# Optimization experiments

Measured on AMD Instinct MI355X. Metric: run time of the kernel, lower is better.

## Reference

```python
import jax, jax.numpy as jnp
import numpy as np

N_NODE = 100_000
N_EDGE = 1_000_000
N_QUERY = 256
N_REL = 200  # embedding table has 2*N_REL+1 = 401 rows
IN_DIM = 64
OUT_DIM = 64
ATTN_DIM = 64


def setup_inputs() -> dict:
    key = jax.random.key(0)
    ks = jax.random.split(key, 12)
    r_idx = jax.random.randint(ks[0], (N_EDGE,), 0, N_QUERY)
    rel = jax.random.randint(ks[1], (N_EDGE,), 0, 2 * N_REL + 1)
    sub = jax.random.randint(ks[2], (N_EDGE,), 0, N_NODE)
    obj = jax.random.randint(ks[3], (N_EDGE,), 0, N_NODE)
    zeros = jnp.zeros((N_EDGE,), dtype=jnp.int32)
    # columns: [r_idx, _, rel, _, sub, obj] matching edges[:,0],[:,2],[:,4],[:,5]
    edges = jnp.stack([r_idx, zeros, rel, zeros, sub, obj], axis=1)
    return {
        "q_sub": jax.random.randint(ks[4], (N_QUERY,), 0, N_NODE),
        "q_rel": jax.random.randint(ks[5], (N_QUERY,), 0, 2 * N_REL + 1),
        "hidden": jax.random.normal(ks[6], (N_NODE, IN_DIM), dtype=jnp.float32),
        "edges": edges,
        "n_node": N_NODE,
        "rela_embed": jax.random.normal(ks[7], (2 * N_REL + 1, IN_DIM), dtype=jnp.float32) * 0.1,
        "Ws": jax.random.normal(ks[8], (IN_DIM, ATTN_DIM), dtype=jnp.float32) * (IN_DIM ** -0.5),
        "Wr": jax.random.normal(ks[9], (IN_DIM, ATTN_DIM), dtype=jnp.float32) * (IN_DIM ** -0.5),
        "Wqr": jax.random.normal(ks[10], (IN_DIM, ATTN_DIM), dtype=jnp.float32) * (IN_DIM ** -0.5),
        "Wqr_b": jnp.zeros((ATTN_DIM,), dtype=jnp.float32),
        "w_alpha_w": jax.random.normal(ks[11], (ATTN_DIM, 1), dtype=jnp.float32) * (ATTN_DIM ** -0.5),
        "w_alpha_b": jnp.zeros((1,), dtype=jnp.float32),
        "W_h": jax.random.normal(jax.random.fold_in(key, 99), (IN_DIM, OUT_DIM), dtype=jnp.float32) * (IN_DIM ** -0.5),
    }


def reference(q_sub, q_rel, hidden, edges, n_node, rela_embed, Ws, Wr, Wqr,
              Wqr_b, w_alpha_w, w_alpha_b, W_h):
    sub = edges[:, 4]
    rel = edges[:, 2]
    obj = edges[:, 5]
    r_idx = edges[:, 0]

    hs = hidden[sub]                    # [E, in_dim] gather
    hr = rela_embed[rel]                # [E, in_dim]
    h_qr = rela_embed[q_rel][r_idx]     # [E, in_dim]

    message = hs + hr                   # [E, in_dim]

    attn = jax.nn.relu(hs @ Ws + hr @ Wr + (h_qr @ Wqr + Wqr_b))  # [E, attn_dim]
    alpha_temp = attn @ w_alpha_w + w_alpha_b                      # [E, 1]
    alpha = jax.nn.sigmoid(alpha_temp)                             # [E, 1]

    message = alpha * message
    message_agg = jax.ops.segment_sum(message, obj, num_segments=n_node)  # [n_node, in_dim]
    hidden_new = message_agg @ W_h      # act is identity (default)
    return hidden_new, alpha, message, obj, alpha_temp
```

## Files before the change

kernel.cpp:

```cpp
#include <hip/hip_runtime.h>
#include <hip/hip_bf16.h>
#include <hip/hip_fp16.h>
#include <cstddef>


typedef float    f32x4 __attribute__((ext_vector_type(4)));
typedef _Float16 f16x8 __attribute__((ext_vector_type(8)));

#define NT_STORE(p, v) __builtin_nontemporal_store((v), (p))

__global__ void fused_pre_kernel(const float* __restrict__ hidden,
                                 const float* __restrict__ Ws,
                                 _Float16* __restrict__ packed, int nnode,
                                 const float* __restrict__ rela,
                                 const float* __restrict__ Wr,
                                 const float* __restrict__ Wqr,
                                 const float* __restrict__ Wqr_b,
                                 const int* __restrict__ q_rel,
                                 _Float16* __restrict__ Br16,
                                 _Float16* __restrict__ Cq16,
                                 _Float16* __restrict__ rela16,
                                 int nrel, int nq,
                                 _Float16* __restrict__ agg,
                                 int mmB, int relB, int zB) {
    __shared__ float W1[64][64];
    __shared__ float W2[64][64];
    int bid = blockIdx.x;
    int tid = threadIdx.x;

    if (bid < mmB) {
        for (int i = tid; i < 4096; i += 256) W1[i >> 6][i & 63] = Ws[i];
        __syncthreads();
        int col = tid & 63, r4 = tid >> 6;
        for (long row = (long)bid * 4 + r4; row < nnode; row += (long)mmB * 4) {
            float xv  = hidden[row * 64 + col];
            float acc = 0.0f;
#pragma unroll
            for (int k = 0; k < 64; ++k)
                acc = fmaf(__shfl(xv, k, 64), W1[k][col], acc);
            packed[row * 128 + col]      = (_Float16)xv;
            packed[row * 128 + 64 + col] = (_Float16)acc;
        }
    } else if (bid < mmB + relB) {
        for (int i = tid; i < 4096; i += 256) {
            W1[i >> 6][i & 63] = Wr[i];
            W2[i >> 6][i & 63] = Wqr[i];
        }
        __syncthreads();
        int col = tid & 63, r4 = tid >> 6;
        int row = (bid - mmB) * 4 + r4;
        int total = nrel + nq;
        if (row < total) {
            if (row < nrel) {
                float xv  = rela[(size_t)row * 64 + col];
                float acc = 0.0f;
#pragma unroll
                for (int k = 0; k < 64; ++k)
                    acc = fmaf(__shfl(xv, k, 64), W1[k][col], acc);
                Br16[(size_t)row * 64 + col]   = (_Float16)acc;
                rela16[(size_t)row * 64 + col] = (_Float16)xv;
            } else {
                int q  = row - nrel;
                int rr = q_rel[q];
                float xv  = rela[(size_t)rr * 64 + col];
                float acc = Wqr_b[col];
#pragma unroll
                for (int k = 0; k < 64; ++k)
                    acc = fmaf(__shfl(xv, k, 64), W2[k][col], acc);
                Cq16[(size_t)q * 64 + col] = (_Float16)acc;
            }
        }
    } else {
        size_t n16 = (size_t)nnode * 8;
        size_t i = (size_t)(bid - mmB - relB) * 256 + tid;
        size_t stride = (size_t)zB * 256;
        f32x4 z = {0.f, 0.f, 0.f, 0.f};
        for (; i < n16; i += stride)
            __builtin_nontemporal_store(z, (f32x4*)agg + i);
    }
}

__global__ void edge_kernel(const int* __restrict__ edges,
                            const _Float16* __restrict__ packed,
                            const _Float16* __restrict__ rela16,
                            const _Float16* __restrict__ Br16,
                            const _Float16* __restrict__ Cq16,
                            const float* __restrict__ w_alpha_w,
                            const float* __restrict__ w_alpha_b,
                            _Float16* __restrict__ agg,
                            float* __restrict__ out_alpha,
                            float* __restrict__ out_message,
                            float* __restrict__ out_obj,
                            float* __restrict__ out_alpha_temp,
                            int nedge) {
    __shared__ __align__(16) _Float16 sm[4][8][64];
    int tid  = threadIdx.x;
    int wv   = tid >> 6;
    int lane = tid & 63;
    int g    = lane >> 3;
    int s    = lane & 7;
    long e0  = ((long)blockIdx.x * 4 + wv) * 8;
    if ((long)blockIdx.x * 32 >= nedge) return;
    long e   = e0 + g;
    bool valid = (e < nedge);

    int md = 0;
    long mbase = e0 * 6;
    if (lane < 48 && (mbase + lane) < (long)nedge * 6) md = edges[mbase + lane];
    int r_idx = __shfl(md, g * 6 + 0, 64);
    int rel   = __shfl(md, g * 6 + 2, 64);
    int sub   = __shfl(md, g * 6 + 4, 64);
    int obj   = __shfl(md, g * 6 + 5, 64);
    if (!valid) { r_idx = 0; rel = 0; sub = 0; obj = 0; }

    const f16x8 hh = *(const f16x8*)(packed + (size_t)sub * 128 + s * 8);
    const f16x8 hw = *(const f16x8*)(packed + (size_t)sub * 128 + 64 + s * 8);
    const f16x8 br = *(const f16x8*)(Br16   + (size_t)rel   * 64 + s * 8);
    const f16x8 cq = *(const f16x8*)(Cq16   + (size_t)r_idx * 64 + s * 8);
    const f16x8 rv = *(const f16x8*)(rela16 + (size_t)rel   * 64 + s * 8);
    const f32x4 wa0 = *(const f32x4*)(w_alpha_w + s * 8);
    const f32x4 wa1 = *(const f32x4*)(w_alpha_w + s * 8 + 4);

    float dot = 0.0f;
#pragma unroll
    for (int j = 0; j < 8; ++j) {
        float a  = fmaxf((float)hw[j] + (float)br[j] + (float)cq[j], 0.0f);
        float wj = (j < 4) ? wa0[j] : wa1[j - 4];
        dot = fmaf(a, wj, dot);
    }
    dot += __shfl_xor(dot, 1, 64);
    dot += __shfl_xor(dot, 2, 64);
    dot += __shfl_xor(dot, 4, 64);

    float at    = dot + w_alpha_b[0];
    float alpha = 1.0f / (1.0f + __expf(-at));

    float m[8];
#pragma unroll
    for (int j = 0; j < 8; ++j)
        m[j] = alpha * ((float)hh[j] + (float)rv[j]);

    if (valid) {
        f32x4 m0 = {m[0], m[1], m[2], m[3]};
        f32x4 m1 = {m[4], m[5], m[6], m[7]};
        __builtin_nontemporal_store(m0, (f32x4*)(out_message + e * 64 + s * 8));
        __builtin_nontemporal_store(m1, (f32x4*)(out_message + e * 64 + s * 8 + 4));
        if (s == 0) {
            NT_STORE(&out_alpha[e], alpha);
            NT_STORE(&out_obj[e], (float)obj);
            NT_STORE(&out_alpha_temp[e], at);
        }
    }

    f16x8 mh;
#pragma unroll
    for (int j = 0; j < 8; ++j) mh[j] = (_Float16)m[j];
    *(f16x8*)&sm[wv][g][s * 8] = mh;
    __syncthreads();
#pragma unroll
    for (int i = 0; i < 4; ++i) {
        int k = 2 * i + (lane >> 5);
        int h = lane & 31;
        if (e0 + k < nedge) {
            __half2 v = *(__half2*)&sm[wv][k][h * 2];
            int ok = __shfl(obj, k * 8, 64);
            unsafeAtomicAdd((__half2*)(agg + (size_t)ok * 64) + h, v);
        }
    }
}

__global__ void matmul64_f16_kernel(const _Float16* __restrict__ X,
                                    const float* __restrict__ W,
                                    float* __restrict__ Y, int nrows) {
    __shared__ float Wl[64][64];
    int tid = threadIdx.x;
    for (int i = tid; i < 4096; i += 256) Wl[i >> 6][i & 63] = W[i];
    __syncthreads();
    int col = tid & 63;
    int r4  = tid >> 6;
    for (long row = (long)blockIdx.x * 4 + r4; row < nrows;
         row += (long)gridDim.x * 4) {
        float xv  = (float)X[row * 64 + col];
        float acc = 0.0f;
#pragma unroll
        for (int k = 0; k < 64; ++k)
            acc = fmaf(__shfl(xv, k, 64), Wl[k][col], acc);
        NT_STORE(&Y[row * 64 + col], acc);
    }
}

extern "C" void kernel_launch(void* const* d_in, const int* in_sizes, int n_in,
                              void* d_out, int out_size, void* d_ws, size_t ws_size,
                              hipStream_t stream) {
    const int*   q_rel     = (const int*)d_in[1];
    const float* hidden    = (const float*)d_in[2];
    const int*   edges     = (const int*)d_in[3];
    const float* rela      = (const float*)d_in[5];
    const float* Ws        = (const float*)d_in[6];
    const float* Wr        = (const float*)d_in[7];
    const float* Wqr       = (const float*)d_in[8];
    const float* Wqr_b     = (const float*)d_in[9];
    const float* w_alpha_w = (const float*)d_in[10];
    const float* w_alpha_b = (const float*)d_in[11];
    const float* W_h       = (const float*)d_in[12];

    const int n_node = in_sizes[2] / 64;
    const int n_edge = in_sizes[3] / 6;
    const int n_rel  = in_sizes[5] / 64;
    const int n_q    = in_sizes[1];

    float* out            = (float*)d_out;
    float* out_hidden_new = out;
    float* out_alpha      = out + (size_t)n_node * 64;
    float* out_message    = out_alpha + n_edge;
    float* out_obj        = out_message + (size_t)n_edge * 64;
    float* out_alpha_temp = out_obj + n_edge;

    _Float16* packed = (_Float16*)d_ws;
    _Float16* agg    = packed + (size_t)n_node * 128;
    _Float16* Br16   = agg + (size_t)n_node * 64;
    _Float16* Cq16   = Br16 + (size_t)n_rel * 64;
    _Float16* rela16 = Cq16 + (size_t)n_q * 64;

    const int mmB  = 2048;
    const int relB = (n_rel + n_q + 3) / 4;
    const int zB   = 512;
    fused_pre_kernel<<<mmB + relB + zB, 256, 0, stream>>>(
        hidden, Ws, packed, n_node,
        rela, Wr, Wqr, Wqr_b, q_rel, Br16, Cq16, rela16, n_rel, n_q,
        agg, mmB, relB, zB);

    {
        int grid = (n_edge + 31) / 32;
        edge_kernel<<<grid, 256, 0, stream>>>(edges, packed, rela16, Br16, Cq16,
                                              w_alpha_w, w_alpha_b, agg,
                                              out_alpha, out_message, out_obj,
                                              out_alpha_temp, n_edge);
    }

    matmul64_f16_kernel<<<2048, 256, 0, stream>>>(agg, W_h, out_hidden_new,
                                                  n_node);
}
```

Measured before the change: 266.8 us.

## Drop edge-kernel block barrier, split rel/query precompute, add dual accumulators

Removes the __syncthreads between the per-wave LDS staging write and the atomic scatter reads in the edge kernel. This relies on each wave only reading its own sm[wv] slice. The Wr and Wqr projections now run in separate block ranges, so each block stages a single 64x64 weight tile and the second shared array is gone. All three 64-wide matvec loops use two independent accumulators for extra ILP. The number of projection blocks for hidden@Ws doubles. Skipping the barrier is correct only if same-wave LDS write-to-read ordering holds, which the code does not enforce explicitly.

```diff
diff --git a/kernel.cpp b/kernel.cpp
--- a/kernel.cpp
+++ b/kernel.cpp
@@ -22,9 +22,8 @@
                                  _Float16* __restrict__ rela16,
                                  int nrel, int nq,
                                  _Float16* __restrict__ agg,
-                                 int mmB, int relB, int zB) {
+                                 int mmB, int brB, int cqB, int zB) {
     __shared__ float W1[64][64];
-    __shared__ float W2[64][64];
     int bid = blockIdx.x;
     int tid = threadIdx.x;
 
@@ -34,45 +33,50 @@
         int col = tid & 63, r4 = tid >> 6;
         for (long row = (long)bid * 4 + r4; row < nnode; row += (long)mmB * 4) {
             float xv  = hidden[row * 64 + col];
-            float acc = 0.0f;
-#pragma unroll
-            for (int k = 0; k < 64; ++k)
-                acc = fmaf(__shfl(xv, k, 64), W1[k][col], acc);
+            float a0 = 0.0f, a1 = 0.0f;
+#pragma unroll
+            for (int k = 0; k < 64; k += 2) {
+                a0 = fmaf(__shfl(xv, k, 64),     W1[k][col],     a0);
+                a1 = fmaf(__shfl(xv, k + 1, 64), W1[k + 1][col], a1);
+            }
             packed[row * 128 + col]      = (_Float16)xv;
-            packed[row * 128 + 64 + col] = (_Float16)acc;
-        }
-    } else if (bid < mmB + relB) {
-        for (int i = tid; i < 4096; i += 256) {
-            W1[i >> 6][i & 63] = Wr[i];
-            W2[i >> 6][i & 63] = Wqr[i];
-        }
+            packed[row * 128 + 64 + col] = (_Float16)(a0 + a1);
+        }
+    } else if (bid < mmB + brB) {
+        for (int i = tid; i < 4096; i += 256) W1[i >> 6][i & 63] = Wr[i];
         __syncthreads();
         int col = tid & 63, r4 = tid >> 6;
         int row = (bid - mmB) * 4 + r4;
-        int total = nrel + nq;
-        if (row < total) {
-            if (row < nrel) {
-                float xv  = rela[(size_t)row * 64 + col];
-                float acc = 0.0f;
-#pragma unroll
-                for (int k = 0; k < 64; ++k)
-                    acc = fmaf(__shfl(xv, k, 64), W1[k][col], acc);
-                Br16[(size_t)row * 64 + col]   = (_Float16)acc;
-                rela16[(size_t)row * 64 + col] = (_Float16)xv;
-            } else {
-                int q  = row - nrel;
-                int rr = q_rel[q];
-                float xv  = rela[(size_t)rr * 64 + col];
-                float acc = Wqr_b[col];
-#pragma unroll
-                for (int k = 0; k < 64; ++k)
-                    acc = fmaf(__shfl(xv, k, 64), W2[k][col], acc);
-                Cq16[(size_t)q * 64 + col] = (_Float16)acc;
+        if (row < nrel) {
+            float xv = rela[(size_t)row * 64 + col];
+            float a0 = 0.0f, a1 = 0.0f;
+#pragma unroll
+            for (int k = 0; k < 64; k += 2) {
+                a0 = fmaf(__shfl(xv, k, 64),     W1[k][col],     a0);
+                a1 = fmaf(__shfl(xv, k + 1, 64), W1[k + 1][col], a1);
             }
+            Br16[(size_t)row * 64 + col]   = (_Float16)(a0 + a1);
+            rela16[(size_t)row * 64 + col] = (_Float16)xv;
+        }
+    } else if (bid < mmB + brB + cqB) {
+        for (int i = tid; i < 4096; i += 256) W1[i >> 6][i & 63] = Wqr[i];
+        __syncthreads();
+        int col = tid & 63, r4 = tid >> 6;
+        int q = (bid - mmB - brB) * 4 + r4;
+        if (q < nq) {
+            int rr = q_rel[q];
+            float xv = rela[(size_t)rr * 64 + col];
+            float a0 = Wqr_b[col], a1 = 0.0f;
+#pragma unroll
+            for (int k = 0; k < 64; k += 2) {
+                a0 = fmaf(__shfl(xv, k, 64),     W1[k][col],     a0);
+                a1 = fmaf(__shfl(xv, k + 1, 64), W1[k + 1][col], a1);
+            }
+            Cq16[(size_t)q * 64 + col] = (_Float16)(a0 + a1);
         }
     } else {
         size_t n16 = (size_t)nnode * 8;
-        size_t i = (size_t)(bid - mmB - relB) * 256 + tid;
+        size_t i = (size_t)(bid - mmB - brB - cqB) * 256 + tid;
         size_t stride = (size_t)zB * 256;
         f32x4 z = {0.f, 0.f, 0.f, 0.f};
         for (; i < n16; i += stride)
@@ -156,7 +160,6 @@
 #pragma unroll
     for (int j = 0; j < 8; ++j) mh[j] = (_Float16)m[j];
     *(f16x8*)&sm[wv][g][s * 8] = mh;
-    __syncthreads();
 #pragma unroll
     for (int i = 0; i < 4; ++i) {
         int k = 2 * i + (lane >> 5);
@@ -181,11 +184,13 @@
     for (long row = (long)blockIdx.x * 4 + r4; row < nrows;
          row += (long)gridDim.x * 4) {
         float xv  = (float)X[row * 64 + col];
-        float acc = 0.0f;
-#pragma unroll
-        for (int k = 0; k < 64; ++k)
-            acc = fmaf(__shfl(xv, k, 64), Wl[k][col], acc);
-        NT_STORE(&Y[row * 64 + col], acc);
+        float a0 = 0.0f, a1 = 0.0f;
+#pragma unroll
+        for (int k = 0; k < 64; k += 2) {
+            a0 = fmaf(__shfl(xv, k, 64),     Wl[k][col],     a0);
+            a1 = fmaf(__shfl(xv, k + 1, 64), Wl[k + 1][col], a1);
+        }
+        NT_STORE(&Y[row * 64 + col], a0 + a1);
     }
 }
 
@@ -222,13 +227,14 @@
     _Float16* Cq16   = Br16 + (size_t)n_rel * 64;
     _Float16* rela16 = Cq16 + (size_t)n_q * 64;
 
-    const int mmB  = 2048;
-    const int relB = (n_rel + n_q + 3) / 4;
-    const int zB   = 512;
-    fused_pre_kernel<<<mmB + relB + zB, 256, 0, stream>>>(
+    const int mmB = 4096;
+    const int brB = (n_rel + 3) / 4;
+    const int cqB = (n_q + 3) / 4;
+    const int zB  = 512;
+    fused_pre_kernel<<<mmB + brB + cqB + zB, 256, 0, stream>>>(
         hidden, Ws, packed, n_node,
         rela, Wr, Wqr, Wqr_b, q_rel, Br16, Cq16, rela16, n_rel, n_q,
-        agg, mmB, relB, zB);
+        agg, mmB, brB, cqB, zB);
 
     {
         int grid = (n_edge + 31) / 32;
```

Result: slower. 274.1 us (+2.7%).
